# Performance work log

Hardware: AMD Instinct MI355X
Metric: run time of the kernel (lower is better)

Reference implementation:

```python
import jax, jax.numpy as jnp
import numpy as np

D = 256      # d_model
H = 8        # nhead
HD = D // H  # head_dim
B = 16       # ragged batch size
L = 4096     # tokens per sample (equal lengths here; code handles general ragged)
NQ = 100     # instance queries per sample


def _xavier(key, shape):
    a = float(np.sqrt(6.0 / (shape[0] + shape[1])))
    return jax.random.uniform(key, shape, jnp.float32, -a, a)


def setup_inputs() -> dict:
    key = jax.random.key(0)
    ks = jax.random.split(key, 8)
    total = B * L
    source = jax.random.normal(ks[0], (total, D), jnp.float32)
    query = jax.random.normal(ks[1], (B, NQ, D), jnp.float32)
    batch_offsets = (jnp.arange(B + 1) * L).astype(jnp.int32)
    # nn.MultiheadAttention params: in-proj (split into q/k/v) + out-proj.
    Wq = _xavier(ks[2], (D, D)); bq = jnp.zeros((D,), jnp.float32)
    Wk = _xavier(ks[3], (D, D)); bk = jnp.zeros((D,), jnp.float32)
    Wv = _xavier(ks[4], (D, D)); bv = jnp.zeros((D,), jnp.float32)
    Wo = _xavier(ks[5], (D, D)); bo = jnp.zeros((D,), jnp.float32)
    return {"source": source, "query": query, "batch_offsets": batch_offsets,
            "Wq": Wq, "bq": bq, "Wk": Wk, "bk": bk, "Wv": Wv, "bv": bv,
            "Wo": Wo, "bo": bo}


def reference(source, query, batch_offsets, Wq, bq, Wk, bk, Wv, bv, Wo, bo):
    # Ragged -> padded gather (indices are concrete, computed with numpy).
    offs = np.asarray(batch_offsets)
    lens = offs[1:] - offs[:-1]                      # (B,)
    Lmax = int(lens.max())
    pos = np.arange(Lmax)
    mask = pos[None, :] < lens[:, None]              # (B, Lmax) valid keys
    idx = np.where(mask, offs[:-1, None] + pos[None, :], 0)
    kv_in = source[jnp.asarray(idx)]                 # (B, Lmax, D)

    # Projections (torch Linear: x @ W.T + b), split into heads.
    q = (query @ Wq.T + bq).reshape(B, NQ, H, HD)
    k = (kv_in @ Wk.T + bk).reshape(B, Lmax, H, HD)
    v = (kv_in @ Wv.T + bv).reshape(B, Lmax, H, HD)

    scale = 1.0 / jnp.sqrt(jnp.asarray(HD, q.dtype))
    scores = jnp.einsum("bqhd,bkhd->bhqk", q * scale, k)
    scores = jnp.where(jnp.asarray(mask)[:, None, None, :], scores, -1e30)
    attn = jax.nn.softmax(scores, axis=-1)           # (B, H, NQ, Lmax)
    ctx = jnp.einsum("bhqk,bkhd->bqhd", attn, v).reshape(B, NQ, D)
    out = ctx @ Wo.T + bo
    # Original code: dropout/norm results are discarded; residual add of query.
    return out + query
```

## Files before the change

### kernel.cpp

```cpp
#include <hip/hip_runtime.h>
#include <hip/hip_bf16.h>
#include <math.h>

#define DM     256
#define NHEAD  8
#define HDIM   32
#define QPAD   112
#define NCHUNK 8
#define BM     64
#define BN     256
#define BK     32

typedef __attribute__((ext_vector_type(8))) short bf16x8;
typedef __attribute__((ext_vector_type(4))) short bf16x4;
typedef __attribute__((ext_vector_type(4))) float f32x4;

__device__ __forceinline__ short f2bf(float f) {
  union { float f; unsigned u; } x; x.f = f;
  unsigned u = (x.u + 0x7fffu + ((x.u >> 16) & 1u)) >> 16;
  return (short)u;
}
__device__ __forceinline__ float bf2f(short s) {
  union { unsigned u; float f; } x; x.u = ((unsigned)(unsigned short)s) << 16;
  return x.f;
}
__device__ __forceinline__ bf16x8 bzero8() {
  bf16x8 v;
#pragma unroll
  for (int j = 0; j < 8; j++) v[j] = (short)0;
  return v;
}
__device__ __forceinline__ void gl2lds16(const void* g, void* l) {
  __builtin_amdgcn_global_load_lds(
      (const __attribute__((address_space(1))) unsigned*)g,
      (__attribute__((address_space(3))) unsigned*)l, 16, 0, 0);
}
__device__ __forceinline__ bf16x8 cvt8(const float* p) {
  float4 x0 = *(const float4*)p, x1 = *(const float4*)(p + 4);
  bf16x8 v;
  v[0] = f2bf(x0.x); v[1] = f2bf(x0.y); v[2] = f2bf(x0.z); v[3] = f2bf(x0.w);
  v[4] = f2bf(x1.x); v[5] = f2bf(x1.y); v[6] = f2bf(x1.z); v[7] = f2bf(x1.w);
  return v;
}

__global__ __launch_bounds__(256) void wconv_kernel(
    const float* __restrict__ Wk, const float* __restrict__ Wv,
    short* __restrict__ Wkv) {
  int idx = blockIdx.x * 256 + threadIdx.x;
  int e0 = idx * 8;
  const float* p = (e0 < DM * DM) ? (Wk + e0) : (Wv + (e0 - DM * DM));
  *(bf16x8*)(Wkv + e0) = cvt8(p);
}

__global__ __launch_bounds__(256) void q_proj_kernel(
    const float* __restrict__ query, const float* __restrict__ Wq,
    const float* __restrict__ bq, short* __restrict__ Qw, int Bn, int NQ) {
  int b  = blockIdx.x / (QPAD / 8);
  int r0 = (blockIdx.x % (QPAD / 8)) * 8;
  __shared__ __align__(16) float ql[8 * DM];
  int tid = threadIdx.x;
  for (int i = tid; i < 8 * DM; i += 256) {
    int r = r0 + (i >> 8);
    ql[i] = (r < NQ) ? query[((size_t)b * NQ + r) * DM + (i & 255)] : 0.f;
  }
  __syncthreads();
  int d = tid;
  float bias = bq[d];
  float acc[8];
#pragma unroll
  for (int qi = 0; qi < 8; qi++) acc[qi] = bias;
  const float* wrow = Wq + (size_t)d * DM;
  for (int k = 0; k < DM; k += 4) {
    float4 w = *(const float4*)(wrow + k);
#pragma unroll
    for (int qi = 0; qi < 8; qi++) {
      float4 x = *(const float4*)&ql[qi * DM + k];
      acc[qi] += x.x * w.x + x.y * w.y + x.z * w.z + x.w * w.w;
    }
  }
  const float scale = 0.17677669529663687f;
  int h = d >> 5, hd = d & 31;
#pragma unroll
  for (int qi = 0; qi < 8; qi++) {
    int r = r0 + qi;
    float v = (r < NQ) ? acc[qi] * scale : 0.f;
    Qw[(((size_t)b * NHEAD + h) * QPAD + r) * HDIM + hd] = f2bf(v);
  }
}

__global__ __launch_bounds__(256) void kv_gemm_kernel(
    const float* __restrict__ src, const short* __restrict__ Wkv,
    const float* __restrict__ bk, const float* __restrict__ bv,
    const int* __restrict__ offs, short* __restrict__ Kw,
    short* __restrict__ Vw, int T, int Bn, int Mtiles) {
  int bid = blockIdx.x;
  int mtile = (bid >> 4) * 8 + (bid & 7);
  int ntile = (bid >> 3) & 1;
  if (mtile >= Mtiles) return;
  int t0 = mtile * BM;
  int n0 = ntile * BN;
  bool isK = (ntile == 0);
  const float* bias = isK ? bk : bv;

  int tid = threadIdx.x;
  int wave = tid >> 6, lane = tid & 63;
  int l15 = lane & 15, quad = lane >> 4;

  __shared__ __align__(16) short As[BM][BK + 8];
  __shared__ __align__(16) short Bs[BN * BK];

  f32x4 acc[4][4];
#pragma unroll
  for (int i = 0; i < 4; i++)
#pragma unroll
    for (int j = 0; j < 4; j++) acc[i][j] = (f32x4){0.f, 0.f, 0.f, 0.f};

  int arow = tid >> 2, ach = tid & 3;
  int atok = t0 + arow;
  if (atok >= T) atok = T - 1;
  const float* asrc = src + (size_t)atok * DM + ach * 8;

  for (int kk = 0; kk < DM; kk += BK) {
    __syncthreads();
    *(bf16x8*)&As[arow][ach * 8] = cvt8(asrc + kk);
    {
      int cloc = lane >> 2;
#pragma unroll
      for (int j = 0; j < 4; j++) {
        int cb = wave * 64 + j * 16;
        int c = cb + cloc;
        int slot = (lane & 3) ^ ((c >> 1) & 3);
        const short* g = Wkv + (size_t)(n0 + c) * DM + kk + slot * 8;
        gl2lds16(g, &Bs[cb * BK]);
      }
    }
    __syncthreads();
    bf16x8 af[4], bf_[4];
#pragma unroll
    for (int mt = 0; mt < 4; mt++)
      af[mt] = *(const bf16x8*)&As[mt * 16 + l15][quad * 8];
#pragma unroll
    for (int nt = 0; nt < 4; nt++) {
      int c = wave * 64 + nt * 16 + l15;
      int slot = quad ^ ((c >> 1) & 3);
      bf_[nt] = *(const bf16x8*)&Bs[c * BK + slot * 8];
    }
    if (isK) {
#pragma unroll
      for (int mt = 0; mt < 4; mt++)
#pragma unroll
        for (int nt = 0; nt < 4; nt++)
          acc[mt][nt] = __builtin_amdgcn_mfma_f32_16x16x32_bf16(
              bf_[nt], af[mt], acc[mt][nt], 0, 0, 0);
    } else {
#pragma unroll
      for (int mt = 0; mt < 4; mt++)
#pragma unroll
        for (int nt = 0; nt < 4; nt++)
          acc[mt][nt] = __builtin_amdgcn_mfma_f32_16x16x32_bf16(
              af[mt], bf_[nt], acc[mt][nt], 0, 0, 0);
    }
  }

  if (isK) {
    float bk4[4][4];
    int hK[4], hdK[4];
#pragma unroll
    for (int nt = 0; nt < 4; nt++) {
      int nbq = wave * 64 + nt * 16 + quad * 4;
      float4 b4 = *(const float4*)(bias + nbq);
      bk4[nt][0] = b4.x; bk4[nt][1] = b4.y; bk4[nt][2] = b4.z; bk4[nt][3] = b4.w;
      hK[nt] = nbq >> 5;
      hdK[nt] = nbq & 31;
    }
    int bcur = 0;
#pragma unroll
    for (int mt = 0; mt < 4; mt++) {
      int tok = t0 + mt * 16 + l15;
      if (tok >= T) continue;
      while (bcur + 1 < Bn && offs[bcur + 1] <= tok) bcur++;
      int off = offs[bcur], len = offs[bcur + 1] - off;
      int l = tok - off;
      size_t bb = (size_t)off * DM;
#pragma unroll
      for (int nt = 0; nt < 4; nt++) {
        bf16x4 p;
#pragma unroll
        for (int r = 0; r < 4; r++) p[r] = f2bf(acc[mt][nt][r] + bk4[nt][r]);
        *(bf16x4*)&Kw[bb + (size_t)hK[nt] * len * HDIM + (size_t)l * HDIM +
                      hdK[nt]] = p;
      }
    }
  } else {
    float bV[4];
    int hV[4], hdV[4];
#pragma unroll
    for (int nt = 0; nt < 4; nt++) {
      int nb = wave * 64 + nt * 16 + l15;
      bV[nt] = bias[nb];
      hV[nt] = nb >> 5;
      hdV[nt] = nb & 31;
    }
    int bcur = 0;
#pragma unroll
    for (int mt = 0; mt < 4; mt++) {
      int tb = t0 + mt * 16 + quad * 4;
      if (tb >= T) continue;
      while (bcur + 1 < Bn && offs[bcur + 1] <= tb) bcur++;
      int off = offs[bcur], len = offs[bcur + 1] - off;
      size_t bb = (size_t)off * DM;
      bool span = (tb + 3 < offs[bcur + 1]) && (tb + 3 < T);
      if (span) {
        int l = tb - off;
#pragma unroll
        for (int nt = 0; nt < 4; nt++) {
          size_t idx =
              bb + (size_t)hV[nt] * len * HDIM + (size_t)hdV[nt] * len + l;
          bf16x4 p;
#pragma unroll
          for (int r = 0; r < 4; r++) p[r] = f2bf(acc[mt][nt][r] + bV[nt]);
          if ((idx & 3) == 0) {
            *(bf16x4*)&Vw[idx] = p;
          } else {
#pragma unroll
            for (int r = 0; r < 4; r++) Vw[idx + r] = p[r];
          }
        }
      } else {
        int bc2 = bcur;
#pragma unroll
        for (int r = 0; r < 4; r++) {
          int tok = tb + r;
          if (tok >= T) continue;
          while (bc2 + 1 < Bn && offs[bc2 + 1] <= tok) bc2++;
          int off2 = offs[bc2], len2 = offs[bc2 + 1] - off2;
          int l = tok - off2;
          size_t bb2 = (size_t)off2 * DM;
#pragma unroll
          for (int nt = 0; nt < 4; nt++)
            Vw[bb2 + (size_t)hV[nt] * len2 * HDIM + (size_t)hdV[nt] * len2 +
               l] = f2bf(acc[mt][nt][r] + bV[nt]);
        }
      }
    }
  }
}

__global__ __launch_bounds__(448) void attn_kernel(
    const short* __restrict__ Qw, const short* __restrict__ Kw,
    const short* __restrict__ Vw, const int* __restrict__ offs,
    short* __restrict__ Ops, float* __restrict__ Ml, int Bn) {
  int c  = blockIdx.x % NCHUNK;
  int bh = blockIdx.x / NCHUNK;
  int h = bh % NHEAD, b = bh / NHEAD;
  int wave = threadIdx.x >> 6, lane = threadIdx.x & 63;
  int l15 = lane & 15, quad = lane >> 4;

  int off = offs[b], len = offs[b + 1] - off;
  int cl = ((len + NCHUNK * 32 - 1) / (NCHUNK * 32)) * 32;
  int kstart = c * cl;
  int kend   = min(kstart + cl, len);

  const short* Kh = Kw + (size_t)off * DM + (size_t)h * len * HDIM;
  const short* Vh = Vw + (size_t)off * DM + (size_t)h * len * HDIM;

  int row16 = wave * 16 + l15;
  bf16x8 aq = *(const bf16x8*)(
      Qw + (((size_t)b * NHEAD + h) * QPAD + row16) * HDIM + quad * 8);

  f32x4 o[2];
#pragma unroll
  for (int j = 0; j < 2; j++) o[j] = (f32x4){0.f, 0.f, 0.f, 0.f};
  float mrun[4], lrun[4];
#pragma unroll
  for (int r = 0; r < 4; r++) { mrun[r] = -1e30f; lrun[r] = 0.f; }

  __shared__ __align__(16) short plds[7][16][40];

  for (int kb = kstart; kb < kend; kb += 32) {
    bool valid[2];
    bf16x8 bk_[2];
#pragma unroll
    for (int nt = 0; nt < 2; nt++) {
      int key = kb + nt * 16 + l15;
      valid[nt] = key < kend;
      bk_[nt] = valid[nt]
                    ? *(const bf16x8*)(Kh + (size_t)key * HDIM + quad * 8)
                    : bzero8();
    }
    f32x4 zero = {0.f, 0.f, 0.f, 0.f};
    f32x4 s[2];
#pragma unroll
    for (int nt = 0; nt < 2; nt++)
      s[nt] = __builtin_amdgcn_mfma_f32_16x16x32_bf16(aq, bk_[nt], zero, 0, 0, 0);
#pragma unroll
    for (int r = 0; r < 4; r++) {
      float v0 = valid[0] ? s[0][r] : -1e30f;
      float v1 = valid[1] ? s[1][r] : -1e30f;
      float t = fmaxf(v0, v1);
      t = fmaxf(t, __shfl_xor(t, 1, 16));
      t = fmaxf(t, __shfl_xor(t, 2, 16));
      t = fmaxf(t, __shfl_xor(t, 4, 16));
      t = fmaxf(t, __shfl_xor(t, 8, 16));
      float mn = fmaxf(mrun[r], t);
      float al = __expf(mrun[r] - mn);
      float p0 = valid[0] ? __expf(v0 - mn) : 0.f;
      float p1 = valid[1] ? __expf(v1 - mn) : 0.f;
      float rs = p0 + p1;
      rs += __shfl_xor(rs, 1, 16);
      rs += __shfl_xor(rs, 2, 16);
      rs += __shfl_xor(rs, 4, 16);
      rs += __shfl_xor(rs, 8, 16);
      lrun[r] = al * lrun[r] + rs;
      mrun[r] = mn;
      o[0][r] *= al;
      o[1][r] *= al;
      plds[wave][quad * 4 + r][l15]      = f2bf(p0);
      plds[wave][quad * 4 + r][16 + l15] = f2bf(p1);
    }
    bf16x8 pa = *(const bf16x8*)&plds[wave][l15][quad * 8];
    bf16x8 bv_[2];
#pragma unroll
    for (int ht = 0; ht < 2; ht++) {
      int hd = ht * 16 + l15;
      int k0 = kb + quad * 8;
      const short* p = Vh + (size_t)hd * len + k0;
      if (k0 + 7 < len) {
        bv_[ht] = *(const bf16x8*)p;
      } else {
        bf16x8 v;
#pragma unroll
        for (int j = 0; j < 8; j++) v[j] = (k0 + j < len) ? p[j] : (short)0;
        bv_[ht] = v;
      }
    }
#pragma unroll
    for (int ht = 0; ht < 2; ht++)
      o[ht] = __builtin_amdgcn_mfma_f32_16x16x32_bf16(pa, bv_[ht], o[ht], 0, 0, 0);
  }

#pragma unroll
  for (int r = 0; r < 4; r++) {
    int row = wave * 16 + quad * 4 + r;
    size_t base = (((size_t)c * Bn + b) * NHEAD + h) * QPAD + row;
#pragma unroll
    for (int ht = 0; ht < 2; ht++)
      Ops[base * HDIM + ht * 16 + l15] = f2bf(o[ht][r]);
    if (l15 == 0) {
      Ml[base * 2]     = mrun[r];
      Ml[base * 2 + 1] = lrun[r];
    }
  }
}

__global__ __launch_bounds__(256) void combine_kernel(
    const short* __restrict__ Ops, const float* __restrict__ Ml,
    const float* __restrict__ query, const float* __restrict__ Wo,
    const float* __restrict__ bo, float* __restrict__ out, int Bn, int NQ) {
  int bpb = (NQ + 7) / 8;
  int b  = blockIdx.x / bpb;
  int q0 = (blockIdx.x % bpb) * 8;
  __shared__ __align__(16) float ctx[8 * DM];
  int d = threadIdx.x;
  int h = d >> 5, hd = d & 31;
#pragma unroll
  for (int qi = 0; qi < 8; qi++) {
    int q = q0 + qi;
    float val = 0.f;
    if (q < NQ) {
      float mc[NCHUNK], lc[NCHUNK], M = -1e30f;
#pragma unroll
      for (int c = 0; c < NCHUNK; c++) {
        size_t base = (((size_t)c * Bn + b) * NHEAD + h) * QPAD + q;
        mc[c] = Ml[base * 2];
        lc[c] = Ml[base * 2 + 1];
        M = fmaxf(M, mc[c]);
      }
      float L = 0.f, acc = 0.f;
#pragma unroll
      for (int c = 0; c < NCHUNK; c++) {
        size_t base = (((size_t)c * Bn + b) * NHEAD + h) * QPAD + q;
        float w = __expf(mc[c] - M);
        L += lc[c] * w;
        acc += w * bf2f(Ops[base * HDIM + hd]);
      }
      val = (L > 0.f) ? acc / L : 0.f;
    }
    ctx[qi * DM + d] = val;
  }
  __syncthreads();
  const float* wrow = Wo + (size_t)d * DM;
  float acc[8];
  float bias = bo[d];
#pragma unroll
  for (int qi = 0; qi < 8; qi++) acc[qi] = bias;
  for (int k = 0; k < DM; k += 4) {
    float4 w = *(const float4*)(wrow + k);
#pragma unroll
    for (int qi = 0; qi < 8; qi++) {
      float4 x = *(const float4*)&ctx[qi * DM + k];
      acc[qi] += x.x * w.x + x.y * w.y + x.z * w.z + x.w * w.w;
    }
  }
#pragma unroll
  for (int qi = 0; qi < 8; qi++) {
    int q = q0 + qi;
    if (q < NQ)
      out[((size_t)b * NQ + q) * DM + d] =
          acc[qi] + query[((size_t)b * NQ + q) * DM + d];
  }
}

extern "C" void kernel_launch(void* const* d_in, const int* in_sizes, int n_in,
                              void* d_out, int out_size, void* d_ws,
                              size_t ws_size, hipStream_t stream) {
  const float* src   = (const float*)d_in[0];
  const float* query = (const float*)d_in[1];
  const int*   offs  = (const int*)d_in[2];
  const float* Wq = (const float*)d_in[3];
  const float* bq = (const float*)d_in[4];
  const float* Wk = (const float*)d_in[5];
  const float* bk = (const float*)d_in[6];
  const float* Wv = (const float*)d_in[7];
  const float* bv = (const float*)d_in[8];
  const float* Wo = (const float*)d_in[9];
  const float* bo = (const float*)d_in[10];
  float* out = (float*)d_out;

  int T  = in_sizes[0] / DM;
  int Bn = in_sizes[2] - 1;
  int NQ = in_sizes[1] / (Bn * DM);

  char* w = (char*)d_ws;
  size_t qsz = (size_t)Bn * NHEAD * QPAD * HDIM * 2;
  size_t ksz = (size_t)T * DM * 2;
  size_t osz = (size_t)NCHUNK * Bn * NHEAD * QPAD * HDIM * 2;
  size_t msz = (size_t)NCHUNK * Bn * NHEAD * QPAD * 2 * 4;
  short* Qw  = (short*)w;
  short* Kw  = (short*)(w + qsz);
  short* Vw  = (short*)(w + qsz + ksz);
  short* Ops = (short*)(w + qsz + 2 * ksz);
  float* Mlp = (float*)(w + qsz + 2 * ksz + osz);
  short* Wkv = (short*)(w + qsz + 2 * ksz + osz + msz);

  int Mtiles = (T + BM - 1) / BM;
  int groups = (Mtiles + 7) / 8;

  wconv_kernel<<<(2 * DM * DM) / (256 * 8), 256, 0, stream>>>(Wk, Wv, Wkv);
  q_proj_kernel<<<Bn * (QPAD / 8), 256, 0, stream>>>(query, Wq, bq, Qw, Bn, NQ);
  kv_gemm_kernel<<<groups * 16, 256, 0, stream>>>(
      src, Wkv, bk, bv, offs, Kw, Vw, T, Bn, Mtiles);
  attn_kernel<<<Bn * NHEAD * NCHUNK, 448, 0, stream>>>(Qw, Kw, Vw, offs, Ops,
                                                       Mlp, Bn);
  combine_kernel<<<Bn * ((NQ + 7) / 8), 256, 0, stream>>>(Ops, Mlp, query, Wo,
                                                          bo, out, Bn, NQ);
}
```

Measured before the change: 273.9 us.

## Stage full A tile in LDS once and read weights directly from global

The KV projection GEMM now converts and stores the whole 64x256 source tile into LDS up front with a padded row stride, removing the per-k-step barriers. The weight tile is no longer staged through LDS via global_load_lds; each wave instead loads its B fragments straight from global memory (cache-resident bf16 weights). This removes the sync and LDS traffic in the k-loop, at the cost of more global/L2 loads per wave and greater LDS use per block.

```diff
diff --git a/kernel.cpp b/kernel.cpp
--- a/kernel.cpp
+++ b/kernel.cpp
@@ -10,6 +10,7 @@
 #define BM     64
 #define BN     256
 #define BK     32
+#define ALD    264
 
 typedef __attribute__((ext_vector_type(8))) short bf16x8;
 typedef __attribute__((ext_vector_type(4))) short bf16x4;
@@ -29,11 +30,6 @@
 #pragma unroll
   for (int j = 0; j < 8; j++) v[j] = (short)0;
   return v;
-}
-__device__ __forceinline__ void gl2lds16(const void* g, void* l) {
-  __builtin_amdgcn_global_load_lds(
-      (const __attribute__((address_space(1))) unsigned*)g,
-      (__attribute__((address_space(3))) unsigned*)l, 16, 0, 0);
 }
 __device__ __forceinline__ bf16x8 cvt8(const float* p) {
   float4 x0 = *(const float4*)p, x1 = *(const float4*)(p + 4);
@@ -106,8 +102,7 @@
   int wave = tid >> 6, lane = tid & 63;
   int l15 = lane & 15, quad = lane >> 4;
 
-  __shared__ __align__(16) short As[BM][BK + 8];
-  __shared__ __align__(16) short Bs[BN * BK];
+  __shared__ __align__(16) short As[BM * ALD];
 
   f32x4 acc[4][4];
 #pragma unroll
@@ -115,36 +110,34 @@
 #pragma unroll
     for (int j = 0; j < 4; j++) acc[i][j] = (f32x4){0.f, 0.f, 0.f, 0.f};
 
-  int arow = tid >> 2, ach = tid & 3;
-  int atok = t0 + arow;
-  if (atok >= T) atok = T - 1;
-  const float* asrc = src + (size_t)atok * DM + ach * 8;
-
+  {
+    int arow = tid >> 2, ac4 = tid & 3;
+    int atok = t0 + arow;
+    if (atok >= T) atok = T - 1;
+    const float* arp = src + (size_t)atok * DM;
+#pragma unroll
+    for (int r = 0; r < 4; r++) {
+      int c0 = r * 64 + ac4 * 16;
+      const float* p = arp + c0;
+      bf16x8 v0 = cvt8(p);
+      bf16x8 v1 = cvt8(p + 8);
+      *(bf16x8*)&As[arow * ALD + c0]     = v0;
+      *(bf16x8*)&As[arow * ALD + c0 + 8] = v1;
+    }
+  }
+  __syncthreads();
+
+  const short* bptr = Wkv + (size_t)(n0 + wave * 64 + l15) * DM + quad * 8;
+#pragma unroll
   for (int kk = 0; kk < DM; kk += BK) {
-    __syncthreads();
-    *(bf16x8*)&As[arow][ach * 8] = cvt8(asrc + kk);
-    {
-      int cloc = lane >> 2;
-#pragma unroll
-      for (int j = 0; j < 4; j++) {
-        int cb = wave * 64 + j * 16;
-        int c = cb + cloc;
-        int slot = (lane & 3) ^ ((c >> 1) & 3);
-        const short* g = Wkv + (size_t)(n0 + c) * DM + kk + slot * 8;
-        gl2lds16(g, &Bs[cb * BK]);
-      }
-    }
-    __syncthreads();
-    bf16x8 af[4], bf_[4];
+    bf16x8 bf_[4];
+#pragma unroll
+    for (int nt = 0; nt < 4; nt++)
+      bf_[nt] = *(const bf16x8*)(bptr + (size_t)nt * 16 * DM + kk);
+    bf16x8 af[4];
 #pragma unroll
     for (int mt = 0; mt < 4; mt++)
-      af[mt] = *(const bf16x8*)&As[mt * 16 + l15][quad * 8];
-#pragma unroll
-    for (int nt = 0; nt < 4; nt++) {
-      int c = wave * 64 + nt * 16 + l15;
-      int slot = quad ^ ((c >> 1) & 3);
-      bf_[nt] = *(const bf16x8*)&Bs[c * BK + slot * 8];
-    }
+      af[mt] = *(const bf16x8*)&As[(mt * 16 + l15) * ALD + kk + quad * 8];
     if (isK) {
 #pragma unroll
       for (int mt = 0; mt < 4; mt++)
```

Measured after the change: 262.5 us. 4.2% less time.
